# Kernel tuning notes

Hardware: AMD Instinct MI355X
Metric: run time of the kernel (lower is better)

The kernel has to match this reference:

```python
import jax, jax.numpy as jnp
import numpy as np

D_IN = 1024
D_OUT = 1024
NUM_HEADS = 16
HEAD_DIM = D_OUT // NUM_HEADS
B = 2
T = 2048


def setup_inputs() -> dict:
    key = jax.random.key(0)
    ks = jax.random.split(key, 6)
    scale = 0.02
    x = jax.random.normal(ks[0], (B, T, D_IN), dtype=jnp.float32)
    Wq = jax.random.normal(ks[1], (D_IN, D_OUT), dtype=jnp.float32) * scale
    Wk = jax.random.normal(ks[2], (D_IN, D_OUT), dtype=jnp.float32) * scale
    Wv = jax.random.normal(ks[3], (D_IN, D_OUT), dtype=jnp.float32) * scale
    Wo = jax.random.normal(ks[4], (D_OUT, D_OUT), dtype=jnp.float32) * scale
    bo = jax.random.normal(ks[5], (D_OUT,), dtype=jnp.float32) * scale
    key_padding_mask = jnp.zeros((B, T), dtype=bool)  # True = padded (masked out)
    return {"x": x, "Wq": Wq, "Wk": Wk, "Wv": Wv, "Wo": Wo, "bo": bo,
            "key_padding_mask": key_padding_mask}


def _mha(x, Wq, Wk, Wv, Wo, bo, key_padding_mask):
    b, t, _ = x.shape
    # projections then split heads: [b, t, H, hd] -> [b, H, t, hd]
    q = (x @ Wq).reshape(b, t, NUM_HEADS, HEAD_DIM).transpose(0, 2, 1, 3)
    k = (x @ Wk).reshape(b, t, NUM_HEADS, HEAD_DIM).transpose(0, 2, 1, 3)
    v = (x @ Wv).reshape(b, t, NUM_HEADS, HEAD_DIM).transpose(0, 2, 1, 3)
    # scores [b, H, t, t]
    scores = jnp.einsum('bhqd,bhkd->bhqk', q, k)
    neg_inf = jnp.float32(-jnp.inf)
    causal = jnp.triu(jnp.ones((t, t), dtype=bool), k=1)  # True above diagonal
    scores = jnp.where(causal[None, None, :, :], neg_inf, scores)
    scores = jnp.where(key_padding_mask[:, None, None, :], neg_inf, scores)
    attn = jax.nn.softmax(scores / np.sqrt(HEAD_DIM).astype(np.float32), axis=-1)
    # dropout p=0.0 -> identity
    ctx = jnp.einsum('bhqk,bhkd->bhqd', attn, v)  # [b, H, t, hd]
    ctx = ctx.transpose(0, 2, 1, 3).reshape(b, t, D_OUT)
    return ctx @ Wo + bo


def reference(x, Wq, Wk, Wv, Wo, bo, key_padding_mask):
    return _mha(x, Wq, Wk, Wv, Wo, bo, key_padding_mask)
```

## Files before the change

### kernel.cpp

```cpp
#include <hip/hip_runtime.h>
#include <math.h>

#define NHEAD 16
#define HD 64
#define BATCH 2
#define TSEQ 2048
#define MTOT (BATCH * TSEQ)
#define DDIM 1024
typedef unsigned short ushort_t;

using short8 = __attribute__((ext_vector_type(8))) short;
using f32x4  = __attribute__((ext_vector_type(4))) float;
using u32x4  = __attribute__((ext_vector_type(4))) unsigned int;
using u32x2  = __attribute__((ext_vector_type(2))) unsigned int;
using u16x4  = __attribute__((ext_vector_type(4))) unsigned short;

#define QSCALE 0.18033688011112042f

static __device__ __forceinline__ ushort_t f2bf(float x) {
    unsigned int u = __builtin_bit_cast(unsigned int, x);
    u += 0x7fff + ((u >> 16) & 1);
    return (ushort_t)(u >> 16);
}
static __device__ __forceinline__ unsigned int pkbf(float a, float b) {
    return __builtin_amdgcn_perm(__builtin_bit_cast(unsigned int, b),
                                 __builtin_bit_cast(unsigned int, a),
                                 0x07060302u);
}
static __device__ __forceinline__ void glds16(const ushort_t* g, ushort_t* l) {
    __builtin_amdgcn_global_load_lds(
        (const __attribute__((address_space(1))) unsigned int*)(g),
        (__attribute__((address_space(3))) unsigned int*)(l), 16, 0, 0);
}

__global__ __launch_bounds__(256)
void convert_x_kernel(const float* __restrict__ X, ushort_t* __restrict__ Xb) {
    int i = (blockIdx.x * 256 + threadIdx.x) * 4;
    f32x4 v = *(const f32x4*)&X[i];
    u16x4 o;
    o.x = f2bf(v.x); o.y = f2bf(v.y); o.z = f2bf(v.z); o.w = f2bf(v.w);
    *(u16x4*)&Xb[i] = o;
}

__global__ __launch_bounds__(256)
void convert_wT_kernel(const float* __restrict__ Wq, const float* __restrict__ Wk,
                       const float* __restrict__ Wv, const float* __restrict__ Wo,
                       ushort_t* __restrict__ Wt) {
    int z = blockIdx.z;
    const float* W = (z == 0) ? Wq : (z == 1) ? Wk : (z == 2) ? Wv : Wo;
    ushort_t* dst = Wt + ((size_t)z << 20);
    __shared__ float tile[32][33];
    int r0 = blockIdx.y * 32, c0 = blockIdx.x * 32;
    int tx = threadIdx.x & 31, ty = threadIdx.x >> 5;
    #pragma unroll
    for (int i = 0; i < 4; ++i)
        tile[ty + i * 8][tx] = W[(size_t)(r0 + ty + i * 8) * DDIM + c0 + tx];
    __syncthreads();
    #pragma unroll
    for (int i = 0; i < 4; ++i)
        dst[(size_t)(c0 + ty + i * 8) * DDIM + r0 + tx] = f2bf(tile[tx][ty + i * 8]);
}

__global__ __launch_bounds__(256)
void qkv_gemm_kernel(const ushort_t* __restrict__ Xb, const ushort_t* __restrict__ Wt,
                     ushort_t* __restrict__ Qb, ushort_t* __restrict__ Kb,
                     ushort_t* __restrict__ Vt) {
    const int bx = blockIdx.x;
    const int z  = bx >> 3;
    const int n0 = (bx & 7) * 128;
    const int m0 = blockIdx.y * 128;
    const ushort_t* Wz = Wt + ((size_t)z << 20);

    __shared__ __align__(16) ushort_t As[128 * 32];
    __shared__ __align__(16) ushort_t Bs[128 * 32];

    const int tid = threadIdx.x;
    const int w = tid >> 6, l = tid & 63, ml = l & 15, q = l >> 4;
    const int wm = (w & 1) * 64, wn = (w >> 1) * 64;

    const int ci0 = tid, ci1 = tid + 256;
    const int ro0 = ci0 >> 2, co0 = (ci0 & 3) * 8;
    const int ro1 = ci1 >> 2, co1 = (ci1 & 3) * 8;
    const ushort_t* ap0 = Xb + (size_t)(m0 + ro0) * DDIM + co0;
    const ushort_t* ap1 = Xb + (size_t)(m0 + ro1) * DDIM + co1;
    const ushort_t* bp0 = Wz + (size_t)(n0 + ro0) * DDIM + co0;
    const ushort_t* bp1 = Wz + (size_t)(n0 + ro1) * DDIM + co1;
    ushort_t* AsW0 = As + w * 512;
    ushort_t* AsW1 = As + 2048 + w * 512;
    ushort_t* BsW0 = Bs + w * 512;
    ushort_t* BsW1 = Bs + 2048 + w * 512;

    f32x4 acc[4][4] = {};

    for (int k0 = 0; k0 < DDIM; k0 += 32) {
        __syncthreads();
        glds16(ap0 + k0, AsW0);
        glds16(ap1 + k0, AsW1);
        glds16(bp0 + k0, BsW0);
        glds16(bp1 + k0, BsW1);
        __syncthreads();
        short8 af[4], bfr[4];
        #pragma unroll
        for (int mi = 0; mi < 4; ++mi)
            af[mi] = *(const short8*)&As[(wm + mi * 16 + ml) * 32 + q * 8];
        #pragma unroll
        for (int ni = 0; ni < 4; ++ni)
            bfr[ni] = *(const short8*)&Bs[(wn + ni * 16 + ml) * 32 + q * 8];
        #pragma unroll
        for (int mi = 0; mi < 4; ++mi)
            #pragma unroll
            for (int ni = 0; ni < 4; ++ni)
                acc[mi][ni] = __builtin_amdgcn_mfma_f32_16x16x32_bf16(
                    af[mi], bfr[ni], acc[mi][ni], 0, 0, 0);
    }

    const float scale = (z == 0) ? QSCALE : 1.0f;
    #pragma unroll
    for (int mi = 0; mi < 4; ++mi) {
        #pragma unroll
        for (int ni = 0; ni < 4; ++ni) {
            #pragma unroll
            for (int r = 0; r < 4; ++r) {
                int mrow = m0 + wm + mi * 16 + q * 4 + r;
                int col  = n0 + wn + ni * 16 + ml;
                int b = mrow >> 11, t = mrow & 2047;
                int head = col >> 6, d = col & 63;
                size_t bh = (size_t)(b * NHEAD + head);
                ushort_t v = f2bf(acc[mi][ni][r] * scale);
                if (z == 0)      Qb[bh * 131072 + (size_t)t * 64 + d] = v;
                else if (z == 1) Kb[bh * 131072 + (size_t)t * 64 + d] = v;
                else             Vt[bh * 131072 + (size_t)d * 2048 + t] = v;
            }
        }
    }
}

__global__ __launch_bounds__(256)
void attn_kernel(const ushort_t* __restrict__ Qb, const ushort_t* __restrict__ Kb,
                 const ushort_t* __restrict__ Vt, ushort_t* __restrict__ ctx) {
    const int p  = blockIdx.x;
    const int bh = blockIdx.y;
    const int pA = p, pB = 31 - p;
    const int tid = threadIdx.x;
    const int w = tid >> 6, l = tid & 63, ml = l & 15, quad = l >> 4;
    const size_t hb = (size_t)bh * 131072;

    __shared__ __align__(16) ushort_t Ps[4 * 2 * 16 * 68];

    const int qA = pA * 64 + w * 16 + ml;
    const int qB = pB * 64 + w * 16 + ml;
    ushort_t* PsA = Ps + (w * 2 + 0) * 1088;
    ushort_t* PsB = Ps + (w * 2 + 1) * 1088;

    short8 bQA[2], bQB[2];
    #pragma unroll
    for (int ss = 0; ss < 2; ++ss) {
        bQA[ss] = *(const short8*)(Qb + hb + (size_t)qA * 64 + ss * 32 + quad * 8);
        bQB[ss] = *(const short8*)(Qb + hb + (size_t)qB * 64 + ss * 32 + quad * 8);
    }

    f32x4 oA[4] = {}, oB[4] = {};
    f32x4 lsA = {}, lsB = {};

    const ushort_t* kp = Kb + hb + (size_t)ml * 64 + quad * 8;
    const ushort_t* vp0 = Vt + hb + (size_t)ml * 2048 + quad * 8;
    const ushort_t* vp1 = vp0 + 16 * 2048;
    const ushort_t* vp2 = vp0 + 32 * 2048;
    const ushort_t* vp3 = vp0 + 48 * 2048;

    auto loadK = [&](short8 (&kf)[4][2]) {
        #pragma unroll
        for (int tk = 0; tk < 4; ++tk)
            #pragma unroll
            for (int ss = 0; ss < 2; ++ss)
                kf[tk][ss] = *(const short8*)(kp + tk * 1024 + ss * 32);
    };

    auto step = [&](int nt, short8 (&kf)[4][2]) {
        const bool actA = (nt <= pA);
        const int n0 = nt * 64;

        short8 vf[4][2];
        #pragma unroll
        for (int ss = 0; ss < 2; ++ss) {
            vf[0][ss] = *(const short8*)(vp0 + ss * 32);
            vf[1][ss] = *(const short8*)(vp1 + ss * 32);
            vf[2][ss] = *(const short8*)(vp2 + ss * 32);
            vf[3][ss] = *(const short8*)(vp3 + ss * 32);
        }
        vp0 += 64; vp1 += 64; vp2 += 64; vp3 += 64;

        f32x4 sA[4], sB[4];
        #pragma unroll
        for (int tk = 0; tk < 4; ++tk) {
            f32x4 zz = {};
            zz = __builtin_amdgcn_mfma_f32_16x16x32_bf16(kf[tk][0], bQB[0], zz, 0, 0, 0);
            zz = __builtin_amdgcn_mfma_f32_16x16x32_bf16(kf[tk][1], bQB[1], zz, 0, 0, 0);
            sB[tk] = zz;
            if (actA) {
                f32x4 za = {};
                za = __builtin_amdgcn_mfma_f32_16x16x32_bf16(kf[tk][0], bQA[0], za, 0, 0, 0);
                za = __builtin_amdgcn_mfma_f32_16x16x32_bf16(kf[tk][1], bQA[1], za, 0, 0, 0);
                sA[tk] = za;
            }
        }

        #pragma unroll
        for (int tk = 0; tk < 4; ++tk) {
            f32x4 pv;
            #pragma unroll
            for (int r = 0; r < 4; ++r) pv[r] = exp2f(sB[tk][r]);
            if (nt == pB) {
                #pragma unroll
                for (int r = 0; r < 4; ++r)
                    if (n0 + tk * 16 + quad * 4 + r > qB) pv[r] = 0.f;
            }
            lsB += pv;
            u32x2 pk; pk.x = pkbf(pv[0], pv[1]); pk.y = pkbf(pv[2], pv[3]);
            *(u32x2*)&PsB[ml * 68 + tk * 16 + quad * 4] = pk;
        }
        if (actA) {
            #pragma unroll
            for (int tk = 0; tk < 4; ++tk) {
                f32x4 pv;
                #pragma unroll
                for (int r = 0; r < 4; ++r) pv[r] = exp2f(sA[tk][r]);
                if (nt == pA) {
                    #pragma unroll
                    for (int r = 0; r < 4; ++r)
                        if (n0 + tk * 16 + quad * 4 + r > qA) pv[r] = 0.f;
                }
                lsA += pv;
                u32x2 pk; pk.x = pkbf(pv[0], pv[1]); pk.y = pkbf(pv[2], pv[3]);
                *(u32x2*)&PsA[ml * 68 + tk * 16 + quad * 4] = pk;
            }
        }

        #pragma unroll
        for (int ss = 0; ss < 2; ++ss) {
            short8 bPB = *(const short8*)&PsB[ml * 68 + ss * 32 + quad * 8];
            short8 bPA;
            if (actA) bPA = *(const short8*)&PsA[ml * 68 + ss * 32 + quad * 8];
            #pragma unroll
            for (int td = 0; td < 4; ++td) {
                oB[td] = __builtin_amdgcn_mfma_f32_16x16x32_bf16(vf[td][ss], bPB, oB[td], 0, 0, 0);
                if (actA)
                    oA[td] = __builtin_amdgcn_mfma_f32_16x16x32_bf16(vf[td][ss], bPA, oA[td], 0, 0, 0);
            }
        }
    };

    short8 k0[4][2], k1[4][2];
    loadK(k0);
    int nt = 0;
    for (;;) {
        if (nt < pB) { kp += 4096; loadK(k1); }
        step(nt, k0);
        if (nt >= pB) break;
        ++nt;
        if (nt < pB) { kp += 4096; loadK(k0); }
        step(nt, k1);
        if (nt >= pB) break;
        ++nt;
    }

    float lA = lsA[0] + lsA[1] + lsA[2] + lsA[3];
    float lB = lsB[0] + lsB[1] + lsB[2] + lsB[3];
    lA += __shfl_xor(lA, 16);  lA += __shfl_xor(lA, 32);
    lB += __shfl_xor(lB, 16);  lB += __shfl_xor(lB, 32);

    const int b = bh >> 4, h = bh & 15;
    {
        float inv = 1.0f / lA;
        size_t rowb = ((size_t)(b * TSEQ + qA)) * DDIM + h * 64;
        #pragma unroll
        for (int td = 0; td < 4; ++td) {
            u16x4 pk;
            pk.x = f2bf(oA[td][0] * inv); pk.y = f2bf(oA[td][1] * inv);
            pk.z = f2bf(oA[td][2] * inv); pk.w = f2bf(oA[td][3] * inv);
            *(u16x4*)&ctx[rowb + td * 16 + quad * 4] = pk;
        }
    }
    {
        float inv = 1.0f / lB;
        size_t rowb = ((size_t)(b * TSEQ + qB)) * DDIM + h * 64;
        #pragma unroll
        for (int td = 0; td < 4; ++td) {
            u16x4 pk;
            pk.x = f2bf(oB[td][0] * inv); pk.y = f2bf(oB[td][1] * inv);
            pk.z = f2bf(oB[td][2] * inv); pk.w = f2bf(oB[td][3] * inv);
            *(u16x4*)&ctx[rowb + td * 16 + quad * 4] = pk;
        }
    }
}

__global__ __launch_bounds__(256)
void out_gemm_kernel(const ushort_t* __restrict__ Cx, const ushort_t* __restrict__ Wt,
                     const float* __restrict__ bo, float* __restrict__ out) {
    const int n0 = blockIdx.x * 64;
    const int m0 = blockIdx.y * 128;
    const ushort_t* Wz = Wt + ((size_t)3 << 20);

    __shared__ __align__(16) ushort_t As[128 * 32];
    __shared__ __align__(16) ushort_t Bs[64 * 32];

    const int tid = threadIdx.x;
    const int w = tid >> 6, l = tid & 63, ml = l & 15, q = l >> 4;
    const int wm = (w & 1) * 64, wn = (w >> 1) * 32;

    const int aro0 = tid >> 2,         aco0 = (tid & 3) * 8;
    const int aro1 = (tid + 256) >> 2, aco1 = (tid & 3) * 8;
    const int bro  = tid >> 2,         bco  = (tid & 3) * 8;
    const ushort_t* ap0 = Cx + (size_t)(m0 + aro0) * DDIM + aco0;
    const ushort_t* ap1 = Cx + (size_t)(m0 + aro1) * DDIM + aco1;
    const ushort_t* bp  = Wz + (size_t)(n0 + bro) * DDIM + bco;
    ushort_t* AsW0 = As + w * 512;
    ushort_t* AsW1 = As + 2048 + w * 512;
    ushort_t* BsW  = Bs + w * 512;

    f32x4 acc[4][2] = {};

    for (int k0 = 0; k0 < DDIM; k0 += 32) {
        __syncthreads();
        glds16(ap0 + k0, AsW0);
        glds16(ap1 + k0, AsW1);
        glds16(bp + k0, BsW);
        __syncthreads();
        short8 af[4], bfr[2];
        #pragma unroll
        for (int mi = 0; mi < 4; ++mi)
            af[mi] = *(const short8*)&As[(wm + mi * 16 + ml) * 32 + q * 8];
        #pragma unroll
        for (int ni = 0; ni < 2; ++ni)
            bfr[ni] = *(const short8*)&Bs[(wn + ni * 16 + ml) * 32 + q * 8];
        #pragma unroll
        for (int mi = 0; mi < 4; ++mi)
            #pragma unroll
            for (int ni = 0; ni < 2; ++ni)
                acc[mi][ni] = __builtin_amdgcn_mfma_f32_16x16x32_bf16(
                    af[mi], bfr[ni], acc[mi][ni], 0, 0, 0);
    }

    #pragma unroll
    for (int mi = 0; mi < 4; ++mi) {
        #pragma unroll
        for (int ni = 0; ni < 2; ++ni) {
            int col = n0 + wn + ni * 16 + ml;
            float bias = bo[col];
            #pragma unroll
            for (int r = 0; r < 4; ++r) {
                int mrow = m0 + wm + mi * 16 + q * 4 + r;
                out[(size_t)mrow * DDIM + col] = acc[mi][ni][r] + bias;
            }
        }
    }
}

extern "C" void kernel_launch(void* const* d_in, const int* in_sizes, int n_in,
                              void* d_out, int out_size, void* d_ws, size_t ws_size,
                              hipStream_t stream)
{
    const float* x  = (const float*)d_in[0];
    const float* Wq = (const float*)d_in[1];
    const float* Wk = (const float*)d_in[2];
    const float* Wv = (const float*)d_in[3];
    const float* Wo = (const float*)d_in[4];
    const float* bo = (const float*)d_in[5];

    char* ws = (char*)d_ws;
    ushort_t* Xb  = (ushort_t*)(ws);
    ushort_t* Wt  = (ushort_t*)(ws + (8u  << 20));
    ushort_t* Qb  = (ushort_t*)(ws + (16u << 20));
    ushort_t* Kb  = (ushort_t*)(ws + (24u << 20));
    ushort_t* Vt  = (ushort_t*)(ws + (32u << 20));
    ushort_t* Cx  = (ushort_t*)(ws + (40u << 20));

    convert_x_kernel<<<dim3(MTOT * DDIM / 1024), 256, 0, stream>>>(x, Xb);
    convert_wT_kernel<<<dim3(32, 32, 4), 256, 0, stream>>>(Wq, Wk, Wv, Wo, Wt);
    qkv_gemm_kernel<<<dim3(24, 32), 256, 0, stream>>>(Xb, Wt, Qb, Kb, Vt);
    attn_kernel<<<dim3(16, 32), 256, 0, stream>>>(Qb, Kb, Vt, Cx);
    out_gemm_kernel<<<dim3(16, 32), 256, 0, stream>>>(Cx, Wt, bo, (float*)d_out);
}
```

Measured before the change: 263.4 us.

## Double-buffer LDS tiles in GEMMs and stage attention K through swizzled LDS

The QKV and output GEMMs now use two LDS buffers. The next K-slice is issued with async global-to-LDS loads while the current slice is consumed, which removes one barrier per iteration and overlaps load latency with MFMA work. The attention kernel drops its register double-buffering of K: each wave loads a slice of the 64-key tile cooperatively into a double-buffered, XOR-swizzled LDS area, and fragments are read back from there. This cuts redundant per-lane global K loads and register pressure, at the cost of a block-wide barrier per key tile and more LDS use.

```diff
diff --git a/kernel.cpp b/kernel.cpp
--- a/kernel.cpp
+++ b/kernel.cpp
@@ -71,8 +71,8 @@
     const int m0 = blockIdx.y * 128;
     const ushort_t* Wz = Wt + ((size_t)z << 20);
 
-    __shared__ __align__(16) ushort_t As[128 * 32];
-    __shared__ __align__(16) ushort_t Bs[128 * 32];
+    __shared__ __align__(16) ushort_t As[2][128 * 32];
+    __shared__ __align__(16) ushort_t Bs[2][128 * 32];
 
     const int tid = threadIdx.x;
     const int w = tid >> 6, l = tid & 63, ml = l & 15, q = l >> 4;
@@ -85,27 +85,30 @@
     const ushort_t* ap1 = Xb + (size_t)(m0 + ro1) * DDIM + co1;
     const ushort_t* bp0 = Wz + (size_t)(n0 + ro0) * DDIM + co0;
     const ushort_t* bp1 = Wz + (size_t)(n0 + ro1) * DDIM + co1;
-    ushort_t* AsW0 = As + w * 512;
-    ushort_t* AsW1 = As + 2048 + w * 512;
-    ushort_t* BsW0 = Bs + w * 512;
-    ushort_t* BsW1 = Bs + 2048 + w * 512;
 
     f32x4 acc[4][4] = {};
 
+    glds16(ap0, As[0] + w * 512);
+    glds16(ap1, As[0] + 2048 + w * 512);
+    glds16(bp0, Bs[0] + w * 512);
+    glds16(bp1, Bs[0] + 2048 + w * 512);
+
     for (int k0 = 0; k0 < DDIM; k0 += 32) {
+        const int cur = (k0 >> 5) & 1;
         __syncthreads();
-        glds16(ap0 + k0, AsW0);
-        glds16(ap1 + k0, AsW1);
-        glds16(bp0 + k0, BsW0);
-        glds16(bp1 + k0, BsW1);
-        __syncthreads();
+        if (k0 + 32 < DDIM) {
+            glds16(ap0 + k0 + 32, As[cur ^ 1] + w * 512);
+            glds16(ap1 + k0 + 32, As[cur ^ 1] + 2048 + w * 512);
+            glds16(bp0 + k0 + 32, Bs[cur ^ 1] + w * 512);
+            glds16(bp1 + k0 + 32, Bs[cur ^ 1] + 2048 + w * 512);
+        }
         short8 af[4], bfr[4];
         #pragma unroll
         for (int mi = 0; mi < 4; ++mi)
-            af[mi] = *(const short8*)&As[(wm + mi * 16 + ml) * 32 + q * 8];
+            af[mi] = *(const short8*)&As[cur][(wm + mi * 16 + ml) * 32 + q * 8];
         #pragma unroll
         for (int ni = 0; ni < 4; ++ni)
-            bfr[ni] = *(const short8*)&Bs[(wn + ni * 16 + ml) * 32 + q * 8];
+            bfr[ni] = *(const short8*)&Bs[cur][(wn + ni * 16 + ml) * 32 + q * 8];
         #pragma unroll
         for (int mi = 0; mi < 4; ++mi)
             #pragma unroll
@@ -145,6 +148,7 @@
     const int w = tid >> 6, l = tid & 63, ml = l & 15, quad = l >> 4;
     const size_t hb = (size_t)bh * 131072;
 
+    __shared__ __align__(16) ushort_t Ks[2 * 4096];
     __shared__ __align__(16) ushort_t Ps[4 * 2 * 16 * 68];
 
     const int qA = pA * 64 + w * 16 + ml;
@@ -162,23 +166,32 @@
     f32x4 oA[4] = {}, oB[4] = {};
     f32x4 lsA = {}, lsB = {};
 
-    const ushort_t* kp = Kb + hb + (size_t)ml * 64 + quad * 8;
+    const int row0 = w * 16 + (l >> 3);
+    const int row1 = row0 + 8;
+    const int c0 = ((l & 7) - row0) & 7;
+    const int c1 = ((l & 7) - row1) & 7;
+    const ushort_t* kgp0 = Kb + hb + (size_t)row0 * 64 + c0 * 8;
+    const ushort_t* kgp1 = Kb + hb + (size_t)row1 * 64 + c1 * 8;
+
+    const int koff0 = ml * 64 + (((0 * 4) + quad + ml) & 7) * 8;
+    const int koff1 = ml * 64 + (((1 * 4) + quad + ml) & 7) * 8;
+
     const ushort_t* vp0 = Vt + hb + (size_t)ml * 2048 + quad * 8;
     const ushort_t* vp1 = vp0 + 16 * 2048;
     const ushort_t* vp2 = vp0 + 32 * 2048;
     const ushort_t* vp3 = vp0 + 48 * 2048;
 
-    auto loadK = [&](short8 (&kf)[4][2]) {
-        #pragma unroll
-        for (int tk = 0; tk < 4; ++tk)
-            #pragma unroll
-            for (int ss = 0; ss < 2; ++ss)
-                kf[tk][ss] = *(const short8*)(kp + tk * 1024 + ss * 32);
-    };
-
-    auto step = [&](int nt, short8 (&kf)[4][2]) {
+    glds16(kgp0, Ks + w * 1024);
+    glds16(kgp1, Ks + w * 1024 + 512);
+    kgp0 += 4096; kgp1 += 4096;
+
+    for (int nt = 0; nt <= pB; ++nt) {
         const bool actA = (nt <= pA);
         const int n0 = nt * 64;
+        const int cur = nt & 1;
+        const ushort_t* KsR = Ks + cur * 4096;
+
+        __syncthreads();
 
         short8 vf[4][2];
         #pragma unroll
@@ -190,17 +203,26 @@
         }
         vp0 += 64; vp1 += 64; vp2 += 64; vp3 += 64;
 
+        if (nt < pB) {
+            ushort_t* KsN = Ks + (cur ^ 1) * 4096 + w * 1024;
+            glds16(kgp0, KsN);
+            glds16(kgp1, KsN + 512);
+            kgp0 += 4096; kgp1 += 4096;
+        }
+
         f32x4 sA[4], sB[4];
         #pragma unroll
         for (int tk = 0; tk < 4; ++tk) {
+            short8 aK0 = *(const short8*)&KsR[tk * 1024 + koff0];
+            short8 aK1 = *(const short8*)&KsR[tk * 1024 + koff1];
             f32x4 zz = {};
-            zz = __builtin_amdgcn_mfma_f32_16x16x32_bf16(kf[tk][0], bQB[0], zz, 0, 0, 0);
-            zz = __builtin_amdgcn_mfma_f32_16x16x32_bf16(kf[tk][1], bQB[1], zz, 0, 0, 0);
+            zz = __builtin_amdgcn_mfma_f32_16x16x32_bf16(aK0, bQB[0], zz, 0, 0, 0);
+            zz = __builtin_amdgcn_mfma_f32_16x16x32_bf16(aK1, bQB[1], zz, 0, 0, 0);
             sB[tk] = zz;
             if (actA) {
                 f32x4 za = {};
-                za = __builtin_amdgcn_mfma_f32_16x16x32_bf16(kf[tk][0], bQA[0], za, 0, 0, 0);
-                za = __builtin_amdgcn_mfma_f32_16x16x32_bf16(kf[tk][1], bQA[1], za, 0, 0, 0);
+                za = __builtin_amdgcn_mfma_f32_16x16x32_bf16(aK0, bQA[0], za, 0, 0, 0);
+                za = __builtin_amdgcn_mfma_f32_16x16x32_bf16(aK1, bQA[1], za, 0, 0, 0);
                 sA[tk] = za;
             }
         }
@@ -248,20 +270,6 @@
                     oA[td] = __builtin_amdgcn_mfma_f32_16x16x32_bf16(vf[td][ss], bPA, oA[td], 0, 0, 0);
             }
         }
-    };
-
-    short8 k0[4][2], k1[4][2];
-    loadK(k0);
-    int nt = 0;
-    for (;;) {
-        if (nt < pB) { kp += 4096; loadK(k1); }
-        step(nt, k0);
-        if (nt >= pB) break;
-        ++nt;
-        if (nt < pB) { kp += 4096; loadK(k0); }
-        step(nt, k1);
-        if (nt >= pB) break;
-        ++nt;
     }
 
     float lA = lsA[0] + lsA[1] + lsA[2] + lsA[3];
@@ -301,8 +309,8 @@
     const int m0 = blockIdx.y * 128;
     const ushort_t* Wz = Wt + ((size_t)3 << 20);
 
-    __shared__ __align__(16) ushort_t As[128 * 32];
-    __shared__ __align__(16) ushort_t Bs[64 * 32];
+    __shared__ __align__(16) ushort_t As[2][128 * 32];
+    __shared__ __align__(16) ushort_t Bs[2][64 * 32];
 
     const int tid = threadIdx.x;
     const int w = tid >> 6, l = tid & 63, ml = l & 15, q = l >> 4;
@@ -314,25 +322,28 @@
     const ushort_t* ap0 = Cx + (size_t)(m0 + aro0) * DDIM + aco0;
     const ushort_t* ap1 = Cx + (size_t)(m0 + aro1) * DDIM + aco1;
     const ushort_t* bp  = Wz + (size_t)(n0 + bro) * DDIM + bco;
-    ushort_t* AsW0 = As + w * 512;
-    ushort_t* AsW1 = As + 2048 + w * 512;
-    ushort_t* BsW  = Bs + w * 512;
 
     f32x4 acc[4][2] = {};
 
+    glds16(ap0, As[0] + w * 512);
+    glds16(ap1, As[0] + 2048 + w * 512);
+    glds16(bp,  Bs[0] + w * 512);
+
     for (int k0 = 0; k0 < DDIM; k0 += 32) {
+        const int cur = (k0 >> 5) & 1;
         __syncthreads();
-        glds16(ap0 + k0, AsW0);
-        glds16(ap1 + k0, AsW1);
-        glds16(bp + k0, BsW);
-        __syncthreads();
+        if (k0 + 32 < DDIM) {
+            glds16(ap0 + k0 + 32, As[cur ^ 1] + w * 512);
+            glds16(ap1 + k0 + 32, As[cur ^ 1] + 2048 + w * 512);
+            glds16(bp + k0 + 32,  Bs[cur ^ 1] + w * 512);
+        }
         short8 af[4], bfr[2];
         #pragma unroll
         for (int mi = 0; mi < 4; ++mi)
-            af[mi] = *(const short8*)&As[(wm + mi * 16 + ml) * 32 + q * 8];
+            af[mi] = *(const short8*)&As[cur][(wm + mi * 16 + ml) * 32 + q * 8];
         #pragma unroll
         for (int ni = 0; ni < 2; ++ni)
-            bfr[ni] = *(const short8*)&Bs[(wn + ni * 16 + ml) * 32 + q * 8];
+            bfr[ni] = *(const short8*)&Bs[cur][(wn + ni * 16 + ml) * 32 + q * 8];
         #pragma unroll
         for (int mi = 0; mi < 4; ++mi)
             #pragma unroll
```

Result: faster. 229.5 us (-12.9%).

## Stage K tiles in shared LDS and launch one query tile per block

Applied to the files above, without the earlier changes.

Each block now handles a single 64-row query tile instead of a pair of tiles at opposite ends of the sequence. Each K tile is loaded once per block into a double-buffered, swizzled LDS buffer using direct global-to-LDS loads; before, every wave loaded K into its own registers. A flat 1024-block grid is remapped so heads are interleaved and long and short causal tiles alternate, and launch bounds request four blocks per CU. This cuts redundant global K traffic and register pressure, at the cost of a block-wide barrier every tile and less explicit load balancing within a block.

```diff
diff --git a/kernel.cpp b/kernel.cpp
--- a/kernel.cpp
+++ b/kernel.cpp
@@ -135,50 +135,55 @@
     }
 }
 
-__global__ __launch_bounds__(256)
+__global__ __launch_bounds__(256, 4)
 void attn_kernel(const ushort_t* __restrict__ Qb, const ushort_t* __restrict__ Kb,
                  const ushort_t* __restrict__ Vt, ushort_t* __restrict__ ctx) {
-    const int p  = blockIdx.x;
-    const int bh = blockIdx.y;
-    const int pA = p, pB = 31 - p;
+    const int i = blockIdx.x;
+    const int g = i >> 8, r = i & 255, s = r >> 3;
+    const int qt = (g & 1) ? (31 - s) : s;
+    const int bh = (r & 7) * 4 + g;
+    const int q0 = qt * 64;
     const int tid = threadIdx.x;
     const int w = tid >> 6, l = tid & 63, ml = l & 15, quad = l >> 4;
     const size_t hb = (size_t)bh * 131072;
 
-    __shared__ __align__(16) ushort_t Ps[4 * 2 * 16 * 68];
-
-    const int qA = pA * 64 + w * 16 + ml;
-    const int qB = pB * 64 + w * 16 + ml;
-    ushort_t* PsA = Ps + (w * 2 + 0) * 1088;
-    ushort_t* PsB = Ps + (w * 2 + 1) * 1088;
-
-    short8 bQA[2], bQB[2];
-    #pragma unroll
-    for (int ss = 0; ss < 2; ++ss) {
-        bQA[ss] = *(const short8*)(Qb + hb + (size_t)qA * 64 + ss * 32 + quad * 8);
-        bQB[ss] = *(const short8*)(Qb + hb + (size_t)qB * 64 + ss * 32 + quad * 8);
-    }
-
-    f32x4 oA[4] = {}, oB[4] = {};
-    f32x4 lsA = {}, lsB = {};
-
-    const ushort_t* kp = Kb + hb + (size_t)ml * 64 + quad * 8;
+    __shared__ __align__(16) ushort_t Ks[2 * 4096];
+    __shared__ __align__(16) ushort_t Ps[4 * 16 * 68];
+
+    const int q = q0 + w * 16 + ml;
+    ushort_t* PsW = Ps + w * 1088;
+
+    short8 bQ[2];
+    #pragma unroll
+    for (int ss = 0; ss < 2; ++ss)
+        bQ[ss] = *(const short8*)(Qb + hb + (size_t)q * 64 + ss * 32 + quad * 8);
+
+    f32x4 o[4] = {};
+    f32x4 ls = {};
+
+    const int row0 = w * 16 + (l >> 3);
+    const int row1 = row0 + 8;
+    const int c0 = ((l & 7) - row0) & 7;
+    const int c1 = ((l & 7) - row1) & 7;
+    const ushort_t* kgp0 = Kb + hb + (size_t)row0 * 64 + c0 * 8;
+    const ushort_t* kgp1 = Kb + hb + (size_t)row1 * 64 + c1 * 8;
+    const int koff0 = ml * 64 + ((quad + ml) & 7) * 8;
+    const int koff1 = ml * 64 + ((4 + quad + ml) & 7) * 8;
+
     const ushort_t* vp0 = Vt + hb + (size_t)ml * 2048 + quad * 8;
     const ushort_t* vp1 = vp0 + 16 * 2048;
     const ushort_t* vp2 = vp0 + 32 * 2048;
     const ushort_t* vp3 = vp0 + 48 * 2048;
 
-    auto loadK = [&](short8 (&kf)[4][2]) {
-        #pragma unroll
-        for (int tk = 0; tk < 4; ++tk)
-            #pragma unroll
-            for (int ss = 0; ss < 2; ++ss)
-                kf[tk][ss] = *(const short8*)(kp + tk * 1024 + ss * 32);
-    };
-
-    auto step = [&](int nt, short8 (&kf)[4][2]) {
-        const bool actA = (nt <= pA);
-        const int n0 = nt * 64;
+    glds16(kgp0, Ks + w * 1024);
+    glds16(kgp1, Ks + w * 1024 + 512);
+    kgp0 += 4096; kgp1 += 4096;
+
+    for (int nt = 0; nt <= qt; ++nt) {
+        const int cur = nt & 1;
+        const ushort_t* KsR = Ks + cur * 4096;
+
+        __syncthreads();
 
         short8 vf[4][2];
         #pragma unroll
@@ -190,107 +195,61 @@
         }
         vp0 += 64; vp1 += 64; vp2 += 64; vp3 += 64;
 
-        f32x4 sA[4], sB[4];
+        if (nt < qt) {
+            ushort_t* KsN = Ks + (cur ^ 1) * 4096 + w * 1024;
+            glds16(kgp0, KsN);
+            glds16(kgp1, KsN + 512);
+            kgp0 += 4096; kgp1 += 4096;
+        }
+
+        f32x4 sv[4];
         #pragma unroll
         for (int tk = 0; tk < 4; ++tk) {
+            short8 aK0 = *(const short8*)&KsR[tk * 1024 + koff0];
+            short8 aK1 = *(const short8*)&KsR[tk * 1024 + koff1];
             f32x4 zz = {};
-            zz = __builtin_amdgcn_mfma_f32_16x16x32_bf16(kf[tk][0], bQB[0], zz, 0, 0, 0);
-            zz = __builtin_amdgcn_mfma_f32_16x16x32_bf16(kf[tk][1], bQB[1], zz, 0, 0, 0);
-            sB[tk] = zz;
-            if (actA) {
-                f32x4 za = {};
-                za = __builtin_amdgcn_mfma_f32_16x16x32_bf16(kf[tk][0], bQA[0], za, 0, 0, 0);
-                za = __builtin_amdgcn_mfma_f32_16x16x32_bf16(kf[tk][1], bQA[1], za, 0, 0, 0);
-                sA[tk] = za;
-            }
+            zz = __builtin_amdgcn_mfma_f32_16x16x32_bf16(aK0, bQ[0], zz, 0, 0, 0);
+            zz = __builtin_amdgcn_mfma_f32_16x16x32_bf16(aK1, bQ[1], zz, 0, 0, 0);
+            sv[tk] = zz;
         }
 
         #pragma unroll
         for (int tk = 0; tk < 4; ++tk) {
             f32x4 pv;
             #pragma unroll
-            for (int r = 0; r < 4; ++r) pv[r] = exp2f(sB[tk][r]);
-            if (nt == pB) {
+            for (int rr = 0; rr < 4; ++rr) pv[rr] = exp2f(sv[tk][rr]);
+            if (nt == qt) {
                 #pragma unroll
-                for (int r = 0; r < 4; ++r)
-                    if (n0 + tk * 16 + quad * 4 + r > qB) pv[r] = 0.f;
+                for (int rr = 0; rr < 4; ++rr)
+                    if (tk * 16 + quad * 4 + rr > w * 16 + ml) pv[rr] = 0.f;
             }
-            lsB += pv;
+            ls += pv;
             u32x2 pk; pk.x = pkbf(pv[0], pv[1]); pk.y = pkbf(pv[2], pv[3]);
-            *(u32x2*)&PsB[ml * 68 + tk * 16 + quad * 4] = pk;
-        }
-        if (actA) {
-            #pragma unroll
-            for (int tk = 0; tk < 4; ++tk) {
-                f32x4 pv;
-                #pragma unroll
-                for (int r = 0; r < 4; ++r) pv[r] = exp2f(sA[tk][r]);
-                if (nt == pA) {
-                    #pragma unroll
-                    for (int r = 0; r < 4; ++r)
-                        if (n0 + tk * 16 + quad * 4 + r > qA) pv[r] = 0.f;
-                }
-                lsA += pv;
-                u32x2 pk; pk.x = pkbf(pv[0], pv[1]); pk.y = pkbf(pv[2], pv[3]);
-                *(u32x2*)&PsA[ml * 68 + tk * 16 + quad * 4] = pk;
-            }
+            *(u32x2*)&PsW[ml * 68 + tk * 16 + quad * 4] = pk;
         }
 
         #pragma unroll
         for (int ss = 0; ss < 2; ++ss) {
-            short8 bPB = *(const short8*)&PsB[ml * 68 + ss * 32 + quad * 8];
-            short8 bPA;
-            if (actA) bPA = *(const short8*)&PsA[ml * 68 + ss * 32 + quad * 8];
-            #pragma unroll
-            for (int td = 0; td < 4; ++td) {
-                oB[td] = __builtin_amdgcn_mfma_f32_16x16x32_bf16(vf[td][ss], bPB, oB[td], 0, 0, 0);
-                if (actA)
-                    oA[td] = __builtin_amdgcn_mfma_f32_16x16x32_bf16(vf[td][ss], bPA, oA[td], 0, 0, 0);
-            }
-        }
-    };
-
-    short8 k0[4][2], k1[4][2];
-    loadK(k0);
-    int nt = 0;
-    for (;;) {
-        if (nt < pB) { kp += 4096; loadK(k1); }
-        step(nt, k0);
-        if (nt >= pB) break;
-        ++nt;
-        if (nt < pB) { kp += 4096; loadK(k0); }
-        step(nt, k1);
-        if (nt >= pB) break;
-        ++nt;
-    }
-
-    float lA = lsA[0] + lsA[1] + lsA[2] + lsA[3];
-    float lB = lsB[0] + lsB[1] + lsB[2] + lsB[3];
-    lA += __shfl_xor(lA, 16);  lA += __shfl_xor(lA, 32);
-    lB += __shfl_xor(lB, 16);  lB += __shfl_xor(lB, 32);
+            short8 bP = *(const short8*)&PsW[ml * 68 + ss * 32 + quad * 8];
+            #pragma unroll
+            for (int td = 0; td < 4; ++td)
+                o[td] = __builtin_amdgcn_mfma_f32_16x16x32_bf16(vf[td][ss], bP, o[td], 0, 0, 0);
+        }
+    }
+
+    float lq = ls[0] + ls[1] + ls[2] + ls[3];
+    lq += __shfl_xor(lq, 16);
+    lq += __shfl_xor(lq, 32);
 
     const int b = bh >> 4, h = bh & 15;
-    {
-        float inv = 1.0f / lA;
-        size_t rowb = ((size_t)(b * TSEQ + qA)) * DDIM + h * 64;
-        #pragma unroll
-        for (int td = 0; td < 4; ++td) {
-            u16x4 pk;
-            pk.x = f2bf(oA[td][0] * inv); pk.y = f2bf(oA[td][1] * inv);
-            pk.z = f2bf(oA[td][2] * inv); pk.w = f2bf(oA[td][3] * inv);
-            *(u16x4*)&ctx[rowb + td * 16 + quad * 4] = pk;
-        }
-    }
-    {
-        float inv = 1.0f / lB;
-        size_t rowb = ((size_t)(b * TSEQ + qB)) * DDIM + h * 64;
-        #pragma unroll
-        for (int td = 0; td < 4; ++td) {
-            u16x4 pk;
-            pk.x = f2bf(oB[td][0] * inv); pk.y = f2bf(oB[td][1] * inv);
-            pk.z = f2bf(oB[td][2] * inv); pk.w = f2bf(oB[td][3] * inv);
-            *(u16x4*)&ctx[rowb + td * 16 + quad * 4] = pk;
-        }
+    float inv = 1.0f / lq;
+    size_t rowb = ((size_t)(b * TSEQ + q)) * DDIM + h * 64;
+    #pragma unroll
+    for (int td = 0; td < 4; ++td) {
+        u16x4 pk;
+        pk.x = f2bf(o[td][0] * inv); pk.y = f2bf(o[td][1] * inv);
+        pk.z = f2bf(o[td][2] * inv); pk.w = f2bf(o[td][3] * inv);
+        *(u16x4*)&ctx[rowb + td * 16 + quad * 4] = pk;
     }
 }
 
@@ -378,6 +337,6 @@
     convert_x_kernel<<<dim3(MTOT * DDIM / 1024), 256, 0, stream>>>(x, Xb);
     convert_wT_kernel<<<dim3(32, 32, 4), 256, 0, stream>>>(Wq, Wk, Wv, Wo, Wt);
     qkv_gemm_kernel<<<dim3(24, 32), 256, 0, stream>>>(Xb, Wt, Qb, Kb, Vt);
-    attn_kernel<<<dim3(16, 32), 256, 0, stream>>>(Qb, Kb, Vt, Cx);
+    attn_kernel<<<dim3(1024), 256, 0, stream>>>(Qb, Kb, Vt, Cx);
     out_gemm_kernel<<<dim3(16, 32), 256, 0, stream>>>(Cx, Wt, bo, (float*)d_out);
 }
```

Measured after the change: 238.2 us. 1.11x faster.
